# Performance work log

Measured on AMD Instinct MI355X. Metric: run time of the kernel, lower is better.

Reference implementation:

```python
import jax, jax.numpy as jnp
import numpy as np

N, H = 8192, 1024

def setup_inputs() -> dict:
    key = jax.random.key(0)
    ks = jax.random.split(key, 7)
    s = 1.0 / np.sqrt(H)
    return {
        "x": jax.random.normal(ks[0], (N, H), dtype=jnp.float32),
        "Wq": jax.random.uniform(ks[1], (H, H), dtype=jnp.float32, minval=-s, maxval=s),
        "bq": jax.random.uniform(ks[2], (H,), dtype=jnp.float32, minval=-s, maxval=s),
        "Wk": jax.random.uniform(ks[3], (H, H), dtype=jnp.float32, minval=-s, maxval=s),
        "bk": jax.random.uniform(ks[4], (H,), dtype=jnp.float32, minval=-s, maxval=s),
        "Wv": jax.random.uniform(ks[5], (H, H), dtype=jnp.float32, minval=-s, maxval=s),
        "bv": jax.random.uniform(ks[6], (H,), dtype=jnp.float32, minval=-s, maxval=s),
    }

def reference(x, Wq, bq, Wk, bk, Wv, bv):
    # q/k/v projections: [N, H]
    q = x @ Wq + bq
    k = x @ Wk + bk
    v = x @ Wv + bv
    # full scores [N, N]; NOTE: original has no 1/sqrt(d) scaling
    scores = q @ k.T
    alpha = jax.nn.softmax(scores, axis=1)
    return alpha @ v
```

## Files before the change

kernel.cpp:

```cpp
#include <hip/hip_runtime.h>
#include <hip/hip_bf16.h>
#include <hip/hip_fp16.h>


typedef _Float16 f16x8 __attribute__((ext_vector_type(8)));
typedef float floatx4 __attribute__((ext_vector_type(4)));
typedef float floatx2 __attribute__((ext_vector_type(2)));

__device__ __forceinline__ unsigned short f2h(float f) {
  __half h = __float2half(f);
  return __builtin_bit_cast(unsigned short, h);
}
__device__ __forceinline__ float h2f(unsigned short u) {
  return __half2float(__builtin_bit_cast(__half, u));
}

__device__ __forceinline__ void async16(const void* g, void* l) {
  __builtin_amdgcn_global_load_lds(
      (__attribute__((address_space(1))) unsigned int*)(g),
      (__attribute__((address_space(3))) unsigned int*)(l),
      16, 0, 0);
}


__global__ __launch_bounds__(256) void conv_f32_f16(const float* __restrict__ in,
                                                    unsigned short* __restrict__ out,
                                                    long n) {
  long i = ((long)blockIdx.x * 256 + threadIdx.x) * 4;
  if (i + 3 < n) {
    float4 f = *(const float4*)(in + i);
    ushort4 o;
    o.x = f2h(f.x); o.y = f2h(f.y); o.z = f2h(f.z); o.w = f2h(f.w);
    *(ushort4*)(out + i) = o;
  }
}

__global__ __launch_bounds__(256) void transpose_f32_f16_3(const float* __restrict__ in0,
                                                           const float* __restrict__ in1,
                                                           const float* __restrict__ in2,
                                                           unsigned short* __restrict__ out,
                                                           int rows, int cols) {
  const float* in = (blockIdx.z == 0) ? in0 : (blockIdx.z == 1) ? in1 : in2;
  unsigned short* o = out + (size_t)blockIdx.z * rows * cols;
  __shared__ float tile[32][33];
  int bx = blockIdx.x * 32;
  int by = blockIdx.y * 32;
  int tx = threadIdx.x & 31, ty = threadIdx.x >> 5;
  #pragma unroll
  for (int yy = ty; yy < 32; yy += 8)
    tile[yy][tx] = in[(size_t)(by + yy) * cols + bx + tx];
  __syncthreads();
  #pragma unroll
  for (int yy = ty; yy < 32; yy += 8)
    o[(size_t)(bx + yy) * rows + by + tx] = f2h(tile[tx][yy]);
}

template <int MODE>
__global__ __launch_bounds__(256, 4)
void gemm_bt(const unsigned short* __restrict__ A,
             const unsigned short* __restrict__ B,
             int M, int Nn, int K,
             const float* __restrict__ b0, const float* __restrict__ b1,
             const float* __restrict__ b2,
             unsigned short* __restrict__ out) {
  if constexpr (MODE == 0) {
    B   += (size_t)blockIdx.z * Nn * K;
    out += (size_t)blockIdx.z * M * Nn;
  }
  const float* bias = (MODE != 0) ? nullptr
                      : (blockIdx.z == 0) ? b0 : (blockIdx.z == 1) ? b1 : b2;
  __shared__ unsigned short As[128 * 32];
  __shared__ unsigned short Bs[128 * 32];
  const int tid  = threadIdx.x;
  const int wave = tid >> 6;
  const int lane = tid & 63;
  const int wm = wave >> 1, wn = wave & 1;
  const int quad = lane >> 4, l16 = lane & 15;
  const long bm = (long)blockIdx.y * 128;
  const long bn = (long)blockIdx.x * 128;

  floatx4 acc[4][4] = {};

  const int srow = wave * 32 + (lane >> 2);
  const int scol = (lane & 3) * 8;
  const unsigned short* gA0 = A + (bm + srow) * (long)K + scol;
  const unsigned short* gA1 = gA0 + 16L * K;
  const unsigned short* gB0 = B + (bn + srow) * (long)K + scol;
  const unsigned short* gB1 = gB0 + 16L * K;
  unsigned short* lA0 = &As[(wave * 32) * 32];
  unsigned short* lA1 = &As[(wave * 32 + 16) * 32];
  unsigned short* lB0 = &Bs[(wave * 32) * 32];
  unsigned short* lB1 = &Bs[(wave * 32 + 16) * 32];

  for (int kk = 0; kk < K; kk += 32) {
    async16(gA0 + kk, lA0);
    async16(gA1 + kk, lA1);
    async16(gB0 + kk, lB0);
    async16(gB1 + kk, lB1);
    __syncthreads();
    f16x8 af[4], bfv[4];
    #pragma unroll
    for (int i = 0; i < 4; ++i) {
      af[i]  = *reinterpret_cast<const f16x8*>(&As[(wm * 64 + i * 16 + l16) * 32 + quad * 8]);
      bfv[i] = *reinterpret_cast<const f16x8*>(&Bs[(wn * 64 + i * 16 + l16) * 32 + quad * 8]);
    }
    #pragma unroll
    for (int i = 0; i < 4; ++i)
      #pragma unroll
      for (int j = 0; j < 4; ++j)
        acc[i][j] = __builtin_amdgcn_mfma_f32_16x16x32_f16(af[i], bfv[j], acc[i][j], 0, 0, 0);
    __syncthreads();
  }

  #pragma unroll
  for (int i = 0; i < 4; ++i) {
    const long row0 = bm + wm * 64 + i * 16 + quad * 4;
    #pragma unroll
    for (int j = 0; j < 4; ++j) {
      const long col = bn + wn * 64 + j * 16 + l16;
      const float cb = (MODE == 0) ? bias[col] : 0.0f;
      #pragma unroll
      for (int r = 0; r < 4; ++r)
        out[(row0 + r) * (long)Nn + col] = f2h(acc[i][j][r] + cb);
    }
  }
}

__global__ __launch_bounds__(256) void softmax_compact(unsigned short* __restrict__ S,
                                                       int* __restrict__ nnz, int n) {
  const int row = blockIdx.x;
  const int tid = threadIdx.x;
  const int lane = tid & 63, w = tid >> 6;
  unsigned short* prow = S + (size_t)row * n;
  const __half* hrow = (const __half*)prow;

  float v[32];
  float m = -1e30f;
  #pragma unroll
  for (int i = 0; i < 32; ++i) {
    v[i] = __half2float(hrow[i * 256 + tid]);
    m = fmaxf(m, v[i]);
  }
  #pragma unroll
  for (int off = 32; off > 0; off >>= 1) m = fmaxf(m, __shfl_down(m, off, 64));
  __shared__ float redm[4];
  __shared__ int cnt;
  if (lane == 0) redm[w] = m;
  if (tid == 0) cnt = 0;
  __syncthreads();
  m = fmaxf(fmaxf(redm[0], redm[1]), fmaxf(redm[2], redm[3]));

  float s = 0.0f;
  #pragma unroll
  for (int i = 0; i < 32; ++i) {
    v[i] = __expf(v[i] - m);
    s += v[i];
  }
  #pragma unroll
  for (int off = 32; off > 0; off >>= 1) s += __shfl_down(s, off, 64);
  __shared__ float reds[4];
  if (lane == 0) reds[w] = s;
  __syncthreads();
  s = reds[0] + reds[1] + reds[2] + reds[3];
  const float inv = 1.0f / s;

  unsigned int* pairs = (unsigned int*)prow;
  const int cap = n / 2;
  #pragma unroll
  for (int i = 0; i < 32; ++i) {
    unsigned short hh = f2h(v[i] * inv);
    if (hh) {
      int p = atomicAdd(&cnt, 1);
      if (p < cap) pairs[p] = ((unsigned int)(i * 256 + tid) << 16) | hh;
    }
  }
  __syncthreads();
  const int c = (cnt < cap) ? cnt : cap;
  const int padded = (c + 7) & ~7;
  if (tid < padded - c) pairs[c + tid] = 0u;
  if (tid == 0) nnz[row] = padded;
}

__global__ __launch_bounds__(256) void pv_sliced(const unsigned short* __restrict__ S,
                                                 const int* __restrict__ nnz,
                                                 const unsigned short* __restrict__ v,
                                                 float* __restrict__ out,
                                                 int n) {
  const int wave = threadIdx.x >> 6;
  const int lane = threadIdx.x & 63;
  const int colbase = blockIdx.x * 128 + lane * 2;
  const unsigned colbyte = (unsigned)colbase * 2;
  const char* __restrict__ vb = (const char*)v;
  const char* __restrict__ sb = (const char*)S;

  for (int r = 0; r < 8; ++r) {
    const int row = blockIdx.y + ((wave << 3) + r) << 8 >> 8;
    (void)row;
    break;
  }

  #pragma unroll 1
  for (int r = 0; r < 8; ++r) {
    const int row = blockIdx.y + ((wave << 3) + r) * 256;
    int craw = nnz[row];
    craw = craw < 0 ? 0 : (craw > 4096 ? 4096 : craw);
    const int cnt = __builtin_amdgcn_readfirstlane(craw);
    const unsigned rowbase = (unsigned)row << 14;
    const unsigned pend = rowbase + 16384 - 32;
    unsigned poff = rowbase;
    uint4 q0 = *(const uint4*)(sb + poff);
    uint4 q1 = *(const uint4*)(sb + poff + 16);
    float a0 = 0.f, a1 = 0.f;
    for (int j = 0; j < cnt; j += 8) {
      const unsigned pn = (poff + 32 <= pend) ? poff + 32 : pend;
      const uint4 n0 = *(const uint4*)(sb + pn);
      const uint4 n1 = *(const uint4*)(sb + pn + 16);
      const unsigned p[8] = {q0.x, q0.y, q0.z, q0.w, q1.x, q1.y, q1.z, q1.w};
      #pragma unroll
      for (int u = 0; u < 8; ++u) {
        const ushort2 vv = *(const ushort2*)(vb + (((p[u] & 0xffff0000u) >> 5) + colbyte));
        const float w = h2f((unsigned short)(p[u] & 0xffffu));
        a0 += w * h2f(vv.x);
        a1 += w * h2f(vv.y);
      }
      q0 = n0; q1 = n1; poff = pn;
    }
    floatx2 o = {a0, a1};
    __builtin_nontemporal_store(o, (floatx2*)(out + ((size_t)row << 10) + colbase));
  }
}

extern "C" void kernel_launch(void* const* d_in, const int* in_sizes, int n_in,
                              void* d_out, int out_size, void* d_ws, size_t ws_size,
                              hipStream_t stream) {
  const int N = 8192, H = 1024;
  const float* x  = (const float*)d_in[0];
  const float* Wq = (const float*)d_in[1];
  const float* bq = (const float*)d_in[2];
  const float* Wk = (const float*)d_in[3];
  const float* bk = (const float*)d_in[4];
  const float* Wv = (const float*)d_in[5];
  const float* bv = (const float*)d_in[6];

  char* p = (char*)d_ws;
  unsigned short* xh  = (unsigned short*)p; p += (size_t)N * H * 2;
  unsigned short* WT  = (unsigned short*)p; p += (size_t)3 * H * H * 2;
  unsigned short* qkv = (unsigned short*)p; p += (size_t)3 * N * H * 2;
  unsigned short* S   = (unsigned short*)p; p += (size_t)N * N * 2;
  int*            nnz = (int*)p;            p += (size_t)N * 4;
  if ((size_t)(p - (char*)d_ws) > ws_size) return;
  unsigned short* qh = qkv;
  unsigned short* kh = qkv + (size_t)N * H;
  unsigned short* vh = qkv + (size_t)2 * N * H;

  conv_f32_f16<<<(N * H / 4 + 255) / 256, 256, 0, stream>>>(x, xh, (long)N * H);
  transpose_f32_f16_3<<<dim3(H / 32, H / 32, 3), 256, 0, stream>>>(Wq, Wk, Wv, WT, H, H);

  gemm_bt<0><<<dim3(H / 128, N / 128, 3), 256, 0, stream>>>(xh, WT, N, H, H,
                                                            bq, bk, bv, qkv);

  gemm_bt<1><<<dim3(N / 128, N / 128), 256, 0, stream>>>(qh, kh, N, N, H,
                                                         nullptr, nullptr, nullptr, S);
  softmax_compact<<<N, 256, 0, stream>>>(S, nnz, N);
  pv_sliced<<<dim3(8, N / 32), 256, 0, stream>>>(S, nnz, vh, (float*)d_out, N);
}
```

Before: 544.0 us.

## Software-pipeline sparse PV gathers with fdot2 math and swizzle score GEMM blocks

The sparse PV kernel now issues the V gathers for the next group of eight pairs one iteration ahead, and reads the pair list two groups ahead, so gather latency overlaps with the accumulation. Pairs of fp16 weights and values are packed with perm and combined with fdot2 instead of separate conversions and FMAs. The per-row loop is also bounded by the real count rather than the row end. The score GEMM (MODE 1) remaps block indices with a stride-8 swizzle to improve L2 reuse. fdot2 changes rounding slightly, and holding more gathers in flight raises register pressure.

```diff
diff --git a/kernel.cpp b/kernel.cpp
--- a/kernel.cpp
+++ b/kernel.cpp
@@ -4,6 +4,7 @@
 
 
 typedef _Float16 f16x8 __attribute__((ext_vector_type(8)));
+typedef _Float16 f16x2 __attribute__((ext_vector_type(2)));
 typedef float floatx4 __attribute__((ext_vector_type(4)));
 typedef float floatx2 __attribute__((ext_vector_type(2)));
 
@@ -13,6 +14,17 @@
 }
 __device__ __forceinline__ float h2f(unsigned short u) {
   return __half2float(__builtin_bit_cast(__half, u));
+}
+
+__device__ __forceinline__ float fdot2(unsigned a, unsigned b, float c) {
+#if __has_builtin(__builtin_amdgcn_fdot2)
+  return __builtin_amdgcn_fdot2(__builtin_bit_cast(f16x2, a),
+                                __builtin_bit_cast(f16x2, b), c, false);
+#else
+  f16x2 av = __builtin_bit_cast(f16x2, a);
+  f16x2 bv = __builtin_bit_cast(f16x2, b);
+  return c + (float)av[0] * (float)bv[0] + (float)av[1] * (float)bv[1];
+#endif
 }
 
 __device__ __forceinline__ void async16(const void* g, void* l) {
@@ -69,6 +81,16 @@
   }
   const float* bias = (MODE != 0) ? nullptr
                       : (blockIdx.z == 0) ? b0 : (blockIdx.z == 1) ? b1 : b2;
+
+  unsigned bx = blockIdx.x, by = blockIdx.y;
+  if constexpr (MODE == 1) {
+    const unsigned nb  = gridDim.x * gridDim.y;
+    const unsigned lin = blockIdx.y * gridDim.x + blockIdx.x;
+    const unsigned swz = (lin & 7u) * (nb >> 3) + (lin >> 3);
+    bx = swz % gridDim.x;
+    by = swz / gridDim.x;
+  }
+
   __shared__ unsigned short As[128 * 32];
   __shared__ unsigned short Bs[128 * 32];
   const int tid  = threadIdx.x;
@@ -76,8 +98,8 @@
   const int lane = tid & 63;
   const int wm = wave >> 1, wn = wave & 1;
   const int quad = lane >> 4, l16 = lane & 15;
-  const long bm = (long)blockIdx.y * 128;
-  const long bn = (long)blockIdx.x * 128;
+  const long bm = (long)by * 128;
+  const long bn = (long)bx * 128;
 
   floatx4 acc[4][4] = {};
 
@@ -193,10 +215,13 @@
   const char* __restrict__ vb = (const char*)v;
   const char* __restrict__ sb = (const char*)S;
 
-  for (int r = 0; r < 8; ++r) {
-    const int row = blockIdx.y + ((wave << 3) + r) << 8 >> 8;
-    (void)row;
-    break;
+#define GOFF(p) ((((p) >> 16) << 11) + colbyte)
+#define GLD(p) (*(const unsigned*)(vb + GOFF(p)))
+#define MATH2(pa, pb, ga, gb)                                                  \
+  {                                                                            \
+    const unsigned w01 = __builtin_amdgcn_perm(pb, pa, 0x05040100u);           \
+    a0 = fdot2(w01, __builtin_amdgcn_perm(gb, ga, 0x05040100u), a0);           \
+    a1 = fdot2(w01, __builtin_amdgcn_perm(gb, ga, 0x07060302u), a1);           \
   }
 
   #pragma unroll 1
@@ -205,29 +230,39 @@
     int craw = nnz[row];
     craw = craw < 0 ? 0 : (craw > 4096 ? 4096 : craw);
     const int cnt = __builtin_amdgcn_readfirstlane(craw);
-    const unsigned rowbase = (unsigned)row << 14;
-    const unsigned pend = rowbase + 16384 - 32;
-    unsigned poff = rowbase;
-    uint4 q0 = *(const uint4*)(sb + poff);
-    uint4 q1 = *(const uint4*)(sb + poff + 16);
     float a0 = 0.f, a1 = 0.f;
-    for (int j = 0; j < cnt; j += 8) {
-      const unsigned pn = (poff + 32 <= pend) ? poff + 32 : pend;
-      const uint4 n0 = *(const uint4*)(sb + pn);
-      const uint4 n1 = *(const uint4*)(sb + pn + 16);
-      const unsigned p[8] = {q0.x, q0.y, q0.z, q0.w, q1.x, q1.y, q1.z, q1.w};
-      #pragma unroll
-      for (int u = 0; u < 8; ++u) {
-        const ushort2 vv = *(const ushort2*)(vb + (((p[u] & 0xffff0000u) >> 5) + colbyte));
-        const float w = h2f((unsigned short)(p[u] & 0xffffu));
-        a0 += w * h2f(vv.x);
-        a1 += w * h2f(vv.y);
+    if (cnt > 0) {
+      const unsigned rowbase = (unsigned)row << 14;
+      const unsigned plast = rowbase + (unsigned)(cnt - 8) * 4;
+      uint4 c0 = *(const uint4*)(sb + rowbase);
+      uint4 c1 = *(const uint4*)(sb + rowbase + 16);
+      unsigned g0 = GLD(c0.x), g1 = GLD(c0.y), g2 = GLD(c0.z), g3 = GLD(c0.w);
+      unsigned g4 = GLD(c1.x), g5 = GLD(c1.y), g6 = GLD(c1.z), g7 = GLD(c1.w);
+      unsigned pn = rowbase + 32 <= plast ? rowbase + 32 : plast;
+      uint4 n0 = *(const uint4*)(sb + pn);
+      uint4 n1 = *(const uint4*)(sb + pn + 16);
+      for (int j = 0; j < cnt; j += 8) {
+        const unsigned h0 = GLD(n0.x), h1 = GLD(n0.y), h2 = GLD(n0.z), h3 = GLD(n0.w);
+        const unsigned h4 = GLD(n1.x), h5 = GLD(n1.y), h6 = GLD(n1.z), h7 = GLD(n1.w);
+        const unsigned pn2 = pn + 32 <= plast ? pn + 32 : plast;
+        const uint4 m0 = *(const uint4*)(sb + pn2);
+        const uint4 m1 = *(const uint4*)(sb + pn2 + 16);
+        MATH2(c0.x, c0.y, g0, g1)
+        MATH2(c0.z, c0.w, g2, g3)
+        MATH2(c1.x, c1.y, g4, g5)
+        MATH2(c1.z, c1.w, g6, g7)
+        c0 = n0; c1 = n1;
+        g0 = h0; g1 = h1; g2 = h2; g3 = h3;
+        g4 = h4; g5 = h5; g6 = h6; g7 = h7;
+        n0 = m0; n1 = m1; pn = pn2;
       }
-      q0 = n0; q1 = n1; poff = pn;
     }
     floatx2 o = {a0, a1};
     __builtin_nontemporal_store(o, (floatx2*)(out + ((size_t)row << 10) + colbase));
   }
+#undef MATH2
+#undef GLD
+#undef GOFF
 }
 
 extern "C" void kernel_launch(void* const* d_in, const int* in_sizes, int n_in,
```

Result: slower. 560.1 us (+3.0%).
